# Kernel tuning notes

Hardware: AMD Instinct MI355X
Metric: run time of the kernel (lower is better)

## Reference

```python
import jax, jax.numpy as jnp
import numpy as np

B, T, I, H = 64, 128, 1024, 4096
NNZ_IH, NNZ_HH = 131072, 262144


def setup_inputs() -> dict:
    key = jax.random.key(0)
    ks = jax.random.split(key, 8)
    x = jax.random.normal(ks[0], (B, T, I), dtype=jnp.float32)
    ih_rows = jax.random.randint(ks[1], (NNZ_IH,), 0, H)
    ih_cols = jax.random.randint(ks[2], (NNZ_IH,), 0, I)
    ih_vals = jax.random.normal(ks[3], (NNZ_IH,), dtype=jnp.float32) * 0.02
    hh_rows = jax.random.randint(ks[4], (NNZ_HH,), 0, H)
    hh_cols = jax.random.randint(ks[5], (NNZ_HH,), 0, H)
    hh_vals = jax.random.normal(ks[6], (NNZ_HH,), dtype=jnp.float32) * 0.02
    hh_bias = jnp.zeros((H,), dtype=jnp.float32)
    return dict(x=x, ih_vals=ih_vals, hh_vals=hh_vals, hh_bias=hh_bias,
                ih_rows=ih_rows, ih_cols=ih_cols, hh_rows=hh_rows, hh_cols=hh_cols)


def _spmm(rows, cols, vals, n_out, m):
    # COO SpMM: out[r, :] = sum_{k: rows[k]==r} vals[k] * m[cols[k], :]
    # (duplicate (r,c) pairs sum, matching torch_sparse.coalesce semantics)
    return jax.ops.segment_sum(vals[:, None] * m[cols], rows, num_segments=n_out)


def reference(x, ih_vals, hh_vals, hh_bias, ih_rows, ih_cols, hh_rows, hh_cols):
    # x: (B, T, I) batch_first -> per-step (I, B) since feature_dim=0
    xt = jnp.transpose(x, (1, 2, 0))  # (T, I, B)
    h0 = jnp.zeros((H, x.shape[0]), dtype=x.dtype)  # zeros init, transposed

    def step(h, x_t):
        pre = (_spmm(ih_rows, ih_cols, ih_vals, H, x_t)      # ih, no bias
               + _spmm(hh_rows, hh_cols, hh_vals, H, h)      # hh
               + hh_bias[:, None])                           # hh bias (H,1)
        h_new = jnp.tanh(pre)                                # nonlinearity (layernorm=Identity)
        return h_new, h_new

    _, hs = jax.lax.scan(step, h0, xt)  # hs: (T, H, B)
    return jnp.transpose(hs, (2, 0, 1))  # (B, T, H)
```

## Files before the change

kernel.cpp:

```cpp
#include <hip/hip_runtime.h>
#include <hip/hip_cooperative_groups.h>
#include <math.h>

namespace cg = cooperative_groups;

#define B_ 64
#define T_ 128
#define I_ 1024
#define H_ 4096
#define XCDS 8

#define RNN_BLOCKS 256
#define RNN_THREADS 1024

#define MAXIT_IH 8

__device__ __forceinline__ unsigned short f2bf(float f) {
    unsigned int u = __float_as_uint(f);
    unsigned int r = (u + 0x7fffu + ((u >> 16) & 1u)) >> 16;
    return (unsigned short)r;
}

__device__ __forceinline__ void load2x16_sc0(const void* p0, const void* p1,
                                             uint4& a, uint4& b) {
    asm volatile(
        "global_load_dwordx4 %0, %2, off sc0\n\t"
        "global_load_dwordx4 %1, %3, off sc0\n\t"
        "s_waitcnt vmcnt(0)"
        : "=&v"(a), "=&v"(b)
        : "v"(p0), "v"(p1));
}

__global__ void transpose_x(const float* __restrict__ x, float* __restrict__ xT2) {
    __shared__ float lds[8][129];
    int t  = blockIdx.z;
    int bg = blockIdx.y;
    int i0 = blockIdx.x * 128;
    int tx = threadIdx.x;
    int ty = threadIdx.y;
    int b = bg * 8 + ty;
    lds[ty][tx] = x[(size_t)b * T_ * I_ + (size_t)t * I_ + i0 + tx];
    __syncthreads();
    int n  = ty * 128 + tx;
    int ii = n >> 3;
    int bs = n & 7;
    xT2[(((size_t)t * 8 + bg) * I_ + i0 + ii) * 8 + bs] = lds[bs][ii];
}

__global__ void hist_rows(const int* __restrict__ rows, int nnz, int* __restrict__ counts) {
    int k = blockIdx.x * blockDim.x + threadIdx.x;
    if (k < nnz) atomicAdd(&counts[rows[k]], 1);
}

__global__ void scan_rows(const int* __restrict__ counts, int* __restrict__ rp, int n) {
    int lane = threadIdx.x;
    int chunk = n / 64;
    int base = lane * chunk;
    int s = 0;
    for (int j = 0; j < chunk; ++j) s += counts[base + j];
    int pre = s;
    for (int off = 1; off < 64; off <<= 1) {
        int up = __shfl_up(pre, off, 64);
        if (lane >= off) pre += up;
    }
    int run = pre - s;
    for (int j = 0; j < chunk; ++j) { rp[base + j] = run; run += counts[base + j]; }
    if (lane == 63) rp[n] = run;
}

__global__ void scatter_pack(const int* __restrict__ rows, const int* __restrict__ cols,
                             const float* __restrict__ vals, int nnz,
                             const int* __restrict__ rp, int* __restrict__ cursor,
                             int2* __restrict__ pack) {
    int k = blockIdx.x * blockDim.x + threadIdx.x;
    if (k < nnz) {
        int r = rows[k];
        int pos = atomicAdd(&cursor[r], 1);
        pack[rp[r] + pos] = make_int2(cols[k], __float_as_int(vals[k]));
    }
}

__global__ __launch_bounds__(1024)
void precompute_ih(const float* __restrict__ xT2,
                   const int* __restrict__ rp, const int2* __restrict__ pack,
                   const float* __restrict__ bias,
                   unsigned short* __restrict__ pre) {
    __shared__ __align__(16) float xs[2][I_ * 8];
    int grp  = blockIdx.y;
    int wave = threadIdx.x >> 6;
    int lane = threadIdx.x & 63;
    int rs = lane >> 3;
    int u  = lane & 7;

    int g = blockIdx.x * 16 + wave;
    int r = g * 8 + rs;
    int hb = rp[r];
    int len = rp[r + 1] - hb;
    int lm = len;
    lm = max(lm, __shfl_xor(lm, 8));
    lm = max(lm, __shfl_xor(lm, 16));
    lm = max(lm, __shfl_xor(lm, 32));
    int lmax = __builtin_amdgcn_readfirstlane(lm);
    float bsv = bias[r];

    int   pcol[MAXIT_IH];
    float pval[MAXIT_IH];
    #pragma unroll
    for (int it = 0; it < MAXIT_IH; ++it) {
        int2 pk = make_int2(0, 0);
        if (it * 8 + u < len) pk = pack[hb + it * 8 + u];
        pcol[it] = pk.x << 5;
        pval[it] = __int_as_float(pk.y);
    }

    {
        const float4* s = (const float4*)(xT2 + ((size_t)0 * 8 + grp) * (I_ * 8));
        float4* d = (float4*)xs[0];
        d[threadIdx.x]        = s[threadIdx.x];
        d[1024 + threadIdx.x] = s[1024 + threadIdx.x];
    }
    __syncthreads();

    for (int t = 0; t < T_; ++t) {
        int cur = t & 1;

        float4 st0, st1;
        bool havenext = (t + 1 < T_);
        if (havenext) {
            const float4* s = (const float4*)(xT2 + ((size_t)(t + 1) * 8 + grp) * (I_ * 8));
            st0 = s[threadIdx.x];
            st1 = s[1024 + threadIdx.x];
        }

        const char* xb = (const char*)xs[cur];
        float a[8];
        #pragma unroll
        for (int j = 0; j < 8; ++j) a[j] = 0.0f;

        #pragma unroll
        for (int it = 0; it < MAXIT_IH; ++it) {
            const float* gp = (const float*)(xb + pcol[it]);
            float4 x0 = *(const float4*)gp;
            float4 x1 = *(const float4*)(gp + 4);
            float v = pval[it];
            a[0] += v * x0.x; a[1] += v * x0.y; a[2] += v * x0.z; a[3] += v * x0.w;
            a[4] += v * x1.x; a[5] += v * x1.y; a[6] += v * x1.z; a[7] += v * x1.w;
        }
        if (lmax > 8 * MAXIT_IH) {
            int kk = hb + 8 * MAXIT_IH + u;
            for (int i = 8 * MAXIT_IH; i < lmax; i += 8, kk += 8) {
                int2 pk = make_int2(0, 0);
                if (i + u < len) pk = pack[kk];
                const float* gp = (const float*)(xb + ((size_t)pk.x << 5));
                float4 x0 = *(const float4*)gp;
                float4 x1 = *(const float4*)(gp + 4);
                float v = __int_as_float(pk.y);
                a[0] += v * x0.x; a[1] += v * x0.y; a[2] += v * x0.z; a[3] += v * x0.w;
                a[4] += v * x1.x; a[5] += v * x1.y; a[6] += v * x1.z; a[7] += v * x1.w;
            }
        }
        #pragma unroll
        for (int off = 1; off <= 4; off <<= 1) {
            #pragma unroll
            for (int j = 0; j < 8; ++j) a[j] += __shfl_xor(a[j], off);
        }
        float sel = (u == 0) ? a[0] : (u == 1) ? a[1] : (u == 2) ? a[2] : (u == 3) ? a[3]
                  : (u == 4) ? a[4] : (u == 5) ? a[5] : (u == 6) ? a[6] : a[7];
        float p = sel + bsv;
        int hf = u >> 2, cc = u & 3;
        pre[((size_t)(grp * 2 + hf) * T_ + t) * (H_ * 4) + (size_t)r * 4 + cc] = f2bf(p);

        if (havenext) {
            float4* d = (float4*)xs[cur ^ 1];
            d[threadIdx.x]        = st0;
            d[1024 + threadIdx.x] = st1;
        }
        __syncthreads();
    }
}

__global__ __launch_bounds__(RNN_THREADS, 1)
void rnn_steps(const int* __restrict__ hhp, const int2* __restrict__ hhpack,
               const unsigned short* __restrict__ pre,
               unsigned short* __restrict__ hg,
               int* __restrict__ regcnt, int* __restrict__ barcnt, int* __restrict__ bargen,
               int* __restrict__ owncnt, int* __restrict__ owngrp,
               float* __restrict__ out) {
    cg::grid_group grid = cg::this_grid();
    __shared__ __align__(16) unsigned short sh[H_ * 4];
    __shared__ int meta[2];

    int tid = threadIdx.x;
    if (tid == 0) {
        int x;
        asm volatile("s_getreg_b32 %0, hwreg(HW_REG_XCC_ID)" : "=s"(x));
        x &= 7;
        int slot = __hip_atomic_fetch_add(&regcnt[x], 1, __ATOMIC_RELAXED,
                                          __HIP_MEMORY_SCOPE_AGENT);
        meta[0] = x;
        meta[1] = slot;
    }
    __syncthreads();
    int xcd  = meta[0];
    int slot = meta[1];
    grid.sync();

    if (blockIdx.x == 0 && tid == 0) {
        int list[XCDS]; int nz = 0;
        for (int j = 0; j < XCDS; ++j) {
            owncnt[j] = 0;
            if (__hip_atomic_load(&regcnt[j], __ATOMIC_RELAXED,
                                  __HIP_MEMORY_SCOPE_AGENT) > 0) list[nz++] = j;
        }
        int rr = 0;
        for (int j = 0; j < XCDS; ++j) {
            int present = __hip_atomic_load(&regcnt[j], __ATOMIC_RELAXED,
                                            __HIP_MEMORY_SCOPE_AGENT) > 0;
            int owner = present ? j : list[rr++ % nz];
            owngrp[owner * 8 + owncnt[owner]] = j;
            owncnt[owner] += 1;
        }
    }
    grid.sync();

    int nblk = __hip_atomic_load(&regcnt[xcd], __ATOMIC_RELAXED, __HIP_MEMORY_SCOPE_AGENT);
    int nown = owncnt[xcd];

    int wave = tid >> 6;
    int lane = tid & 63;
    int rs   = lane >> 3;
    int u    = lane & 7;

    int hfbeg, hfend, mywave, nwh;
    if (nblk >= 2) {
        int hf = slot & 1;
        hfbeg = hf; hfend = hf + 1;
        int nhb = (hf == 0) ? ((nblk + 1) >> 1) : (nblk >> 1);
        mywave = (slot >> 1) * (RNN_THREADS / 64) + wave;
        nwh = nhb * (RNN_THREADS / 64);
    } else {
        hfbeg = 0; hfend = 2;
        mywave = wave; nwh = RNN_THREADS / 64;
    }

    int* bc = &barcnt[xcd * 32];
    int* bgen = &bargen[xcd * 32];

    for (int t = 0; t < T_; ++t) {
        for (int oi = 0; oi < nown; ++oi) {
            int grp = owngrp[xcd * 8 + oi];
            for (int hf = hfbeg; hf < hfend; ++hf) {
                const unsigned short* src =
                    hg + (size_t)((grp * 2 + (t & 1)) * 2 + hf) * (H_ * 4);
                unsigned short* dst =
                    hg + (size_t)((grp * 2 + ((t + 1) & 1)) * 2 + hf) * (H_ * 4);

                __syncthreads();
                {
                    uint4 v0, v1;
                    const char* s = (const char*)src;
                    load2x16_sc0(s + (size_t)tid * 16,
                                 s + (size_t)(1024 + tid) * 16, v0, v1);
                    uint4* s4 = (uint4*)sh;
                    s4[tid]        = v0;
                    s4[1024 + tid] = v1;
                }
                __syncthreads();

                for (int g = mywave; g < H_ / 8; g += nwh) {
                    int r  = g * 8 + rs;
                    int hb = hhp[r], he = hhp[r + 1];
                    int len = he - hb;
                    int lmax = len;
                    lmax = max(lmax, __shfl_xor(lmax, 8));
                    lmax = max(lmax, __shfl_xor(lmax, 16));
                    lmax = max(lmax, __shfl_xor(lmax, 32));

                    unsigned short pus =
                        pre[((size_t)(grp * 2 + hf) * T_ + t) * (H_ * 4) +
                            (size_t)r * 4 + u];

                    float a0 = 0.f, a1 = 0.f, a2 = 0.f, a3 = 0.f;
                    int kk = hb + u;
                    int2 pk = make_int2(0, 0);
                    if (u < len) pk = hhpack[kk];
                    for (int i = 0; i < lmax; i += 8) {
                        kk += 8;
                        int2 pkn = make_int2(0, 0);
                        if (i + 8 + u < len) pkn = hhpack[kk];
                        uint2 hw = *(const uint2*)((const char*)sh + ((size_t)pk.x << 3));
                        float v = __int_as_float(pk.y);
                        a0 += v * __uint_as_float(hw.x << 16);
                        a1 += v * __uint_as_float(hw.x & 0xffff0000u);
                        a2 += v * __uint_as_float(hw.y << 16);
                        a3 += v * __uint_as_float(hw.y & 0xffff0000u);
                        pk = pkn;
                    }
                    #pragma unroll
                    for (int off = 1; off <= 4; off <<= 1) {
                        a0 += __shfl_xor(a0, off);
                        a1 += __shfl_xor(a1, off);
                        a2 += __shfl_xor(a2, off);
                        a3 += __shfl_xor(a3, off);
                    }
                    if (u < 4) {
                        float acc = (u == 0) ? a0 : (u == 1) ? a1 : (u == 2) ? a2 : a3;
                        float pv = __uint_as_float((unsigned int)pus << 16);
                        float h = tanhf(acc + pv);
                        dst[(size_t)r * 4 + u] = f2bf(h);
                        int b = grp * 8 + hf * 4 + u;
                        out[(size_t)b * T_ * H_ + (size_t)t * H_ + r] = h;
                    }
                }
            }
        }

        __syncthreads();
        if (tid == 0) {
            asm volatile("s_waitcnt vmcnt(0)" ::: "memory");
            int target = t + 1;
            int old = __hip_atomic_fetch_add(bc, 1, __ATOMIC_RELAXED,
                                             __HIP_MEMORY_SCOPE_AGENT);
            if (old == nblk - 1) {
                __hip_atomic_store(bc, 0, __ATOMIC_RELAXED, __HIP_MEMORY_SCOPE_AGENT);
                __hip_atomic_store(bgen, target, __ATOMIC_RELAXED, __HIP_MEMORY_SCOPE_AGENT);
            } else {
                while (__hip_atomic_load(bgen, __ATOMIC_RELAXED,
                                         __HIP_MEMORY_SCOPE_AGENT) < target) {
                    __builtin_amdgcn_s_sleep(1);
                }
            }
        }
        __syncthreads();
    }
}

extern "C" void kernel_launch(void* const* d_in, const int* in_sizes, int n_in,
                              void* d_out, int out_size, void* d_ws, size_t ws_size,
                              hipStream_t stream) {
    const float* x       = (const float*)d_in[0];
    const float* ih_vals = (const float*)d_in[1];
    const float* hh_vals = (const float*)d_in[2];
    const float* hh_bias = (const float*)d_in[3];
    const int*   ih_rows = (const int*)d_in[4];
    const int*   ih_cols = (const int*)d_in[5];
    const int*   hh_rows = (const int*)d_in[6];
    const int*   hh_cols = (const int*)d_in[7];
    float* out = (float*)d_out;

    const int nnz_ih = in_sizes[1];
    const int nnz_hh = in_sizes[2];

    char* ws = (char*)d_ws;
    size_t off = 0;
    auto alloc = [&](size_t bytes) -> void* {
        off = (off + 255) & ~(size_t)255;
        void* p = ws + off;
        off += bytes;
        return p;
    };

    float* xT2   = (float*)alloc((size_t)T_ * 8 * I_ * 8 * sizeof(float));
    int*   ih_rp = (int*)  alloc((H_ + 1) * sizeof(int));
    int*   hh_rp = (int*)  alloc((H_ + 1) * sizeof(int));

    const int ZINTS = 4 * H_ + 64 + 8 * 32 + 8 * 32 + 8 + 64;
    int* zbase  = (int*)alloc((size_t)ZINTS * sizeof(int));
    int* ih_cnt = zbase;
    int* ih_cur = zbase + H_;
    int* hh_cnt = zbase + 2 * H_;
    int* hh_cur = zbase + 3 * H_;
    int* regcnt = zbase + 4 * H_;
    int* barcnt = regcnt + 64;
    int* bargen = barcnt + 8 * 32;
    int* owncnt = bargen + 8 * 32;
    int* owngrp = owncnt + 8;

    int2* ih_pack = (int2*)alloc((size_t)nnz_ih * sizeof(int2));
    int2* hh_pack = (int2*)alloc((size_t)nnz_hh * sizeof(int2));
    unsigned short* hg = (unsigned short*)alloc((size_t)XCDS * 2 * 2 * H_ * 4 * sizeof(unsigned short));
    unsigned short* pre = (unsigned short*)alloc((size_t)16 * T_ * H_ * 4 * sizeof(unsigned short));

    hipMemsetAsync(zbase, 0, (size_t)ZINTS * sizeof(int), stream);
    hipMemsetAsync(hg, 0, (size_t)XCDS * 2 * 2 * H_ * 4 * sizeof(unsigned short), stream);

    transpose_x<<<dim3(I_ / 128, 8, T_), dim3(128, 8), 0, stream>>>(x, xT2);

    hist_rows<<<(nnz_ih + 255) / 256, 256, 0, stream>>>(ih_rows, nnz_ih, ih_cnt);
    scan_rows<<<1, 64, 0, stream>>>(ih_cnt, ih_rp, H_);
    scatter_pack<<<(nnz_ih + 255) / 256, 256, 0, stream>>>(ih_rows, ih_cols, ih_vals, nnz_ih,
                                                           ih_rp, ih_cur, ih_pack);
    hist_rows<<<(nnz_hh + 255) / 256, 256, 0, stream>>>(hh_rows, nnz_hh, hh_cnt);
    scan_rows<<<1, 64, 0, stream>>>(hh_cnt, hh_rp, H_);
    scatter_pack<<<(nnz_hh + 255) / 256, 256, 0, stream>>>(hh_rows, hh_cols, hh_vals, nnz_hh,
                                                           hh_rp, hh_cur, hh_pack);

    precompute_ih<<<dim3(H_ / 8 / 16, 8), dim3(1024), 0, stream>>>(xT2, ih_rp, ih_pack,
                                                                   hh_bias, pre);

    void* kargs[] = {
        (void*)&hh_rp, (void*)&hh_pack,
        (void*)&pre,
        (void*)&hg,
        (void*)&regcnt, (void*)&barcnt, (void*)&bargen,
        (void*)&owncnt, (void*)&owngrp,
        (void*)&out,
    };
    hipLaunchCooperativeKernel((const void*)rnn_steps, dim3(RNN_BLOCKS), dim3(RNN_THREADS),
                               kargs, 0, stream);
}
```

Baseline: 1.516 ms.

## Store transposed x in bf16 and pad hh CSR rows to uniform group length

The transposed input x is now stored and staged in LDS as bf16 rather than fp32. This halves the global and shared-memory traffic in the ih precompute and shrinks its LDS footprint. Separately, the hh CSR rows are zero-padded so all 8 rows of a group share one length that is a multiple of 8. That removes the per-row bounds checks and shuffle-max from the recurrent inner loop. The cost is lower input precision and a larger, memset-zeroed hh pack buffer.

```diff
diff --git a/kernel.cpp b/kernel.cpp
--- a/kernel.cpp
+++ b/kernel.cpp
@@ -31,7 +31,7 @@
         : "v"(p0), "v"(p1));
 }
 
-__global__ void transpose_x(const float* __restrict__ x, float* __restrict__ xT2) {
+__global__ void transpose_x(const float* __restrict__ x, unsigned short* __restrict__ xT2) {
     __shared__ float lds[8][129];
     int t  = blockIdx.z;
     int bg = blockIdx.y;
@@ -44,12 +44,23 @@
     int n  = ty * 128 + tx;
     int ii = n >> 3;
     int bs = n & 7;
-    xT2[(((size_t)t * 8 + bg) * I_ + i0 + ii) * 8 + bs] = lds[bs][ii];
+    xT2[(((size_t)t * 8 + bg) * I_ + i0 + ii) * 8 + bs] = f2bf(lds[bs][ii]);
 }
 
 __global__ void hist_rows(const int* __restrict__ rows, int nnz, int* __restrict__ counts) {
     int k = blockIdx.x * blockDim.x + threadIdx.x;
     if (k < nnz) atomicAdd(&counts[rows[k]], 1);
+}
+
+__global__ void pad_counts(const int* __restrict__ cnt, int* __restrict__ pcnt) {
+    int grp = blockIdx.x * blockDim.x + threadIdx.x;
+    if (grp >= H_ / 8) return;
+    int m = 0;
+    #pragma unroll
+    for (int j = 0; j < 8; ++j) m = max(m, cnt[grp * 8 + j]);
+    m = (m + 7) & ~7;
+    #pragma unroll
+    for (int j = 0; j < 8; ++j) pcnt[grp * 8 + j] = m;
 }
 
 __global__ void scan_rows(const int* __restrict__ counts, int* __restrict__ rp, int n) {
@@ -81,11 +92,11 @@
 }
 
 __global__ __launch_bounds__(1024)
-void precompute_ih(const float* __restrict__ xT2,
+void precompute_ih(const unsigned short* __restrict__ xT2,
                    const int* __restrict__ rp, const int2* __restrict__ pack,
                    const float* __restrict__ bias,
                    unsigned short* __restrict__ pre) {
-    __shared__ __align__(16) float xs[2][I_ * 8];
+    __shared__ __align__(16) unsigned short xs[2][I_ * 8];
     int grp  = blockIdx.y;
     int wave = threadIdx.x >> 6;
     int lane = threadIdx.x & 63;
@@ -109,27 +120,24 @@
     for (int it = 0; it < MAXIT_IH; ++it) {
         int2 pk = make_int2(0, 0);
         if (it * 8 + u < len) pk = pack[hb + it * 8 + u];
-        pcol[it] = pk.x << 5;
+        pcol[it] = pk.x << 4;
         pval[it] = __int_as_float(pk.y);
     }
 
     {
-        const float4* s = (const float4*)(xT2 + ((size_t)0 * 8 + grp) * (I_ * 8));
-        float4* d = (float4*)xs[0];
-        d[threadIdx.x]        = s[threadIdx.x];
-        d[1024 + threadIdx.x] = s[1024 + threadIdx.x];
+        const uint4* s = (const uint4*)(xT2 + ((size_t)0 * 8 + grp) * (I_ * 8));
+        ((uint4*)xs[0])[threadIdx.x] = s[threadIdx.x];
     }
     __syncthreads();
 
     for (int t = 0; t < T_; ++t) {
         int cur = t & 1;
 
-        float4 st0, st1;
+        uint4 st0;
         bool havenext = (t + 1 < T_);
         if (havenext) {
-            const float4* s = (const float4*)(xT2 + ((size_t)(t + 1) * 8 + grp) * (I_ * 8));
+            const uint4* s = (const uint4*)(xT2 + ((size_t)(t + 1) * 8 + grp) * (I_ * 8));
             st0 = s[threadIdx.x];
-            st1 = s[1024 + threadIdx.x];
         }
 
         const char* xb = (const char*)xs[cur];
@@ -139,24 +147,32 @@
 
         #pragma unroll
         for (int it = 0; it < MAXIT_IH; ++it) {
-            const float* gp = (const float*)(xb + pcol[it]);
-            float4 x0 = *(const float4*)gp;
-            float4 x1 = *(const float4*)(gp + 4);
+            uint4 xw = *(const uint4*)(xb + pcol[it]);
             float v = pval[it];
-            a[0] += v * x0.x; a[1] += v * x0.y; a[2] += v * x0.z; a[3] += v * x0.w;
-            a[4] += v * x1.x; a[5] += v * x1.y; a[6] += v * x1.z; a[7] += v * x1.w;
+            a[0] += v * __uint_as_float(xw.x << 16);
+            a[1] += v * __uint_as_float(xw.x & 0xffff0000u);
+            a[2] += v * __uint_as_float(xw.y << 16);
+            a[3] += v * __uint_as_float(xw.y & 0xffff0000u);
+            a[4] += v * __uint_as_float(xw.z << 16);
+            a[5] += v * __uint_as_float(xw.z & 0xffff0000u);
+            a[6] += v * __uint_as_float(xw.w << 16);
+            a[7] += v * __uint_as_float(xw.w & 0xffff0000u);
         }
         if (lmax > 8 * MAXIT_IH) {
             int kk = hb + 8 * MAXIT_IH + u;
             for (int i = 8 * MAXIT_IH; i < lmax; i += 8, kk += 8) {
                 int2 pk = make_int2(0, 0);
                 if (i + u < len) pk = pack[kk];
-                const float* gp = (const float*)(xb + ((size_t)pk.x << 5));
-                float4 x0 = *(const float4*)gp;
-                float4 x1 = *(const float4*)(gp + 4);
+                uint4 xw = *(const uint4*)(xb + ((size_t)pk.x << 4));
                 float v = __int_as_float(pk.y);
-                a[0] += v * x0.x; a[1] += v * x0.y; a[2] += v * x0.z; a[3] += v * x0.w;
-                a[4] += v * x1.x; a[5] += v * x1.y; a[6] += v * x1.z; a[7] += v * x1.w;
+                a[0] += v * __uint_as_float(xw.x << 16);
+                a[1] += v * __uint_as_float(xw.x & 0xffff0000u);
+                a[2] += v * __uint_as_float(xw.y << 16);
+                a[3] += v * __uint_as_float(xw.y & 0xffff0000u);
+                a[4] += v * __uint_as_float(xw.z << 16);
+                a[5] += v * __uint_as_float(xw.z & 0xffff0000u);
+                a[6] += v * __uint_as_float(xw.w << 16);
+                a[7] += v * __uint_as_float(xw.w & 0xffff0000u);
             }
         }
         #pragma unroll
@@ -171,9 +187,7 @@
         pre[((size_t)(grp * 2 + hf) * T_ + t) * (H_ * 4) + (size_t)r * 4 + cc] = f2bf(p);
 
         if (havenext) {
-            float4* d = (float4*)xs[cur ^ 1];
-            d[threadIdx.x]        = st0;
-            d[1024 + threadIdx.x] = st1;
+            ((uint4*)xs[cur ^ 1])[threadIdx.x] = st0;
         }
         __syncthreads();
     }
@@ -269,12 +283,8 @@
 
                 for (int g = mywave; g < H_ / 8; g += nwh) {
                     int r  = g * 8 + rs;
-                    int hb = hhp[r], he = hhp[r + 1];
-                    int len = he - hb;
-                    int lmax = len;
-                    lmax = max(lmax, __shfl_xor(lmax, 8));
-                    lmax = max(lmax, __shfl_xor(lmax, 16));
-                    lmax = max(lmax, __shfl_xor(lmax, 32));
+                    int hb = hhp[r];
+                    int len = hhp[r + 1] - hb;
 
                     unsigned short pus =
                         pre[((size_t)(grp * 2 + hf) * T_ + t) * (H_ * 4) +
@@ -282,12 +292,10 @@
 
                     float a0 = 0.f, a1 = 0.f, a2 = 0.f, a3 = 0.f;
                     int kk = hb + u;
-                    int2 pk = make_int2(0, 0);
-                    if (u < len) pk = hhpack[kk];
-                    for (int i = 0; i < lmax; i += 8) {
+                    int2 pk = hhpack[kk];
+                    for (int i = 0; i < len; i += 8) {
                         kk += 8;
-                        int2 pkn = make_int2(0, 0);
-                        if (i + 8 + u < len) pkn = hhpack[kk];
+                        int2 pkn = hhpack[kk];
                         uint2 hw = *(const uint2*)((const char*)sh + ((size_t)pk.x << 3));
                         float v = __int_as_float(pk.y);
                         a0 += v * __uint_as_float(hw.x << 16);
@@ -360,9 +368,10 @@
         return p;
     };
 
-    float* xT2   = (float*)alloc((size_t)T_ * 8 * I_ * 8 * sizeof(float));
-    int*   ih_rp = (int*)  alloc((H_ + 1) * sizeof(int));
-    int*   hh_rp = (int*)  alloc((H_ + 1) * sizeof(int));
+    unsigned short* xT2 = (unsigned short*)alloc((size_t)T_ * 8 * I_ * 8 * sizeof(unsigned short));
+    int*   ih_rp  = (int*)alloc((H_ + 1) * sizeof(int));
+    int*   hh_rp  = (int*)alloc((H_ + 1) * sizeof(int));
+    int*   hh_pcnt = (int*)alloc(H_ * sizeof(int));
 
     const int ZINTS = 4 * H_ + 64 + 8 * 32 + 8 * 32 + 8 + 64;
     int* zbase  = (int*)alloc((size_t)ZINTS * sizeof(int));
@@ -377,12 +386,14 @@
     int* owngrp = owncnt + 8;
 
     int2* ih_pack = (int2*)alloc((size_t)nnz_ih * sizeof(int2));
-    int2* hh_pack = (int2*)alloc((size_t)nnz_hh * sizeof(int2));
+    size_t hh_pack_n = (size_t)2 * nnz_hh + 64;
+    int2* hh_pack = (int2*)alloc(hh_pack_n * sizeof(int2));
     unsigned short* hg = (unsigned short*)alloc((size_t)XCDS * 2 * 2 * H_ * 4 * sizeof(unsigned short));
     unsigned short* pre = (unsigned short*)alloc((size_t)16 * T_ * H_ * 4 * sizeof(unsigned short));
 
     hipMemsetAsync(zbase, 0, (size_t)ZINTS * sizeof(int), stream);
     hipMemsetAsync(hg, 0, (size_t)XCDS * 2 * 2 * H_ * 4 * sizeof(unsigned short), stream);
+    hipMemsetAsync(hh_pack, 0, hh_pack_n * sizeof(int2), stream);
 
     transpose_x<<<dim3(I_ / 128, 8, T_), dim3(128, 8), 0, stream>>>(x, xT2);
 
@@ -391,7 +402,8 @@
     scatter_pack<<<(nnz_ih + 255) / 256, 256, 0, stream>>>(ih_rows, ih_cols, ih_vals, nnz_ih,
                                                            ih_rp, ih_cur, ih_pack);
     hist_rows<<<(nnz_hh + 255) / 256, 256, 0, stream>>>(hh_rows, nnz_hh, hh_cnt);
-    scan_rows<<<1, 64, 0, stream>>>(hh_cnt, hh_rp, H_);
+    pad_counts<<<(H_ / 8 + 255) / 256, 256, 0, stream>>>(hh_cnt, hh_pcnt);
+    scan_rows<<<1, 64, 0, stream>>>(hh_pcnt, hh_rp, H_);
     scatter_pack<<<(nnz_hh + 255) / 256, 256, 0, stream>>>(hh_rows, hh_cols, hh_vals, nnz_hh,
                                                            hh_rp, hh_cur, hh_pack);
 
```

Result: faster. 1.439 ms (-5.1%).
